# Kernel tuning notes

Hardware: AMD Instinct MI355X
Metric: run time of the kernel (lower is better)

The kernel has to match this reference:

```python
import jax, jax.numpy as jnp
import numpy as np
import math

B, S, N, D_IN = 32, 60, 25, 100
GRU, TEMB, SEMB, SEM_IN, CH, OUT, NH = 512, 512, 512, 768, 256, 512, 8


def _ln(x, g, b, eps=1e-5):
    m = jnp.mean(x, axis=-1, keepdims=True)
    v = jnp.mean((x - m) ** 2, axis=-1, keepdims=True)
    return (x - m) * jax.lax.rsqrt(v + eps) * g + b


def _gru_dir(x, w_ih, w_hh, b_ih, b_hh, reverse):
    # x: [BN, S, F]; PyTorch GRU gate order (r, z, n); returns final hidden [BN, H]
    H = w_hh.shape[1]
    gi_all = jnp.einsum('bsf,gf->bsg', x, w_ih) + b_ih  # precompute input-side gates

    def step(h, gi):
        gh = h @ w_hh.T + b_hh
        i_r, i_z, i_n = jnp.split(gi, 3, axis=-1)
        h_r, h_z, h_n = jnp.split(gh, 3, axis=-1)
        r = jax.nn.sigmoid(i_r + h_r)
        z = jax.nn.sigmoid(i_z + h_z)
        n = jnp.tanh(i_n + r * h_n)
        h_new = (1.0 - z) * n + z * h
        return h_new, None

    h0 = jnp.zeros((x.shape[0], H), x.dtype)
    h_last, _ = jax.lax.scan(step, h0, jnp.swapaxes(gi_all, 0, 1), reverse=reverse)
    return h_last


def _forward(x, seq1_w1, seq1_b1, seq1_w2, seq1_b2, ln2_g, ln2_b,
             gru_wih_f, gru_whh_f, gru_bih_f, gru_bhh_f,
             gru_wih_b, gru_whh_b, gru_bih_b, gru_bhh_b,
             ln_g, ln_b, attn_in_w, attn_in_b, fc_ta_w, fc_ta_b,
             ln3_g, ln3_b, semantic_embs, sem_w, sem_b, lnsem_g, lnsem_b,
             att_alpha, dist_adj,
             gcn_w0, gcn_b0, gcn_w1, gcn_b1, gcn_w2, gcn_b2,
             gln1_g, gln1_b, gln2_g, gln2_b,
             enc_ln_g, enc_ln_b, fc_w, fc_b):
    Bx, Sx, Nx, _ = x.shape
    # --- latent_correlation_layer ---
    xr = jnp.transpose(x, (0, 2, 1, 3)).reshape(Bx * Nx, Sx, -1)  # [BN,S,D]
    h = jax.nn.relu(xr @ seq1_w1 + seq1_b1)
    h = jax.nn.relu(h @ seq1_w2 + seq1_b2)  # dropout p=0
    h = _ln(h, ln2_g, ln2_b)  # [BN,S,512]
    hf = _gru_dir(h, gru_wih_f, gru_whh_f, gru_bih_f, gru_bhh_f, False)
    hb = _gru_dir(h, gru_wih_b, gru_whh_b, gru_bih_b, gru_bhh_b, True)
    hn = jnp.concatenate([hf, hb], axis=-1).reshape(Bx, Nx, 2 * GRU)
    hn = _ln(hn, ln_g, ln_b)  # [B,N,2*GRU]
    # multihead self-attention weights (averaged over heads, then over batch)
    hd = (2 * GRU) // NH
    qkv = hn @ attn_in_w.T + attn_in_b
    q, k, _v = jnp.split(qkv, 3, axis=-1)
    q = q.reshape(Bx, Nx, NH, hd)
    k = k.reshape(Bx, Nx, NH, hd)
    scores = jnp.einsum('bihd,bjhd->bhij', q, k) / math.sqrt(hd)
    attention = jax.nn.softmax(scores, axis=-1).mean(axis=1).mean(axis=0)  # [N,N]
    # --- node features ---
    wr = jax.nn.relu(hn @ fc_ta_w + fc_ta_b)
    X = _ln(wr, ln3_g, ln3_b)  # [B,N,TEMB]
    te = _ln(semantic_embs @ sem_w + sem_b, lnsem_g, lnsem_b)  # [N,SEMB]
    X = jnp.concatenate([X, jnp.broadcast_to(te, (Bx,) + te.shape)], axis=-1)  # [B,N,TEMB+SEMB]
    # cosine-similarity embedding attention (same for every batch element)
    en = te / jnp.maximum(jnp.linalg.norm(te, axis=-1, keepdims=True), 1e-8)
    embed_att = en @ en.T  # [N,N]
    attention = (att_alpha * dist_adj + (1.0 - att_alpha) * embed_att) * attention
    # case-amplification mask (detached in the original -> stop_gradient)
    m = jax.lax.stop_gradient(attention)
    m = jnp.maximum(m, 0.0) ** 2.5
    m = m / jnp.max(m)
    mask = (m >= 0.08).astype(x.dtype)
    adj = attention * mask
    # --- GCN block (GCNConv, add_self_loops=False, normalize=False, dense adjacency) ---
    def gcn(Xin, W, b):
        # out[i] = sum_j adj[j,i] * (Xin[j] @ W) + b  (source->target flow)
        return jnp.einsum('ji,bjf->bif', adj, Xin @ W) + b
    Xg = jax.nn.relu(gcn(X, gcn_w0, gcn_b0))
    Xg = jax.nn.relu(_ln(gcn(Xg, gcn_w1, gcn_b1) + Xg, gln1_g, gln1_b))
    Xg = jax.nn.relu(_ln(gcn(Xg, gcn_w2, gcn_b2) + Xg, gln2_g, gln2_b))
    # --- encoder head ---
    Xg = _ln(Xg, enc_ln_g, enc_ln_b)
    X_hat = jax.nn.relu(jnp.concatenate([X, Xg], axis=-1) @ fc_w + fc_b)  # [B,N,OUT]
    return X_hat


def setup_inputs():
    key = jax.random.key(0)
    c = [0]

    def nrm(shape, scale=1.0):
        c[0] += 1
        return (jax.random.normal(jax.random.fold_in(key, c[0]), shape) * scale).astype(jnp.float32)

    z = lambda *s: jnp.zeros(s, jnp.float32)
    o = lambda *s: jnp.ones(s, jnp.float32)
    FDIM = TEMB + SEMB
    d = {
        'x': nrm((B, S, N, D_IN)),
        'seq1_w1': nrm((D_IN, 256), 0.06), 'seq1_b1': z(256),
        'seq1_w2': nrm((256, 512), 0.05), 'seq1_b2': z(512),
        'ln2_g': o(512), 'ln2_b': z(512),
        'gru_wih_f': nrm((3 * GRU, 512), 0.04), 'gru_whh_f': nrm((3 * GRU, GRU), 0.04),
        'gru_bih_f': z(3 * GRU), 'gru_bhh_f': z(3 * GRU),
        'gru_wih_b': nrm((3 * GRU, 512), 0.04), 'gru_whh_b': nrm((3 * GRU, GRU), 0.04),
        'gru_bih_b': z(3 * GRU), 'gru_bhh_b': z(3 * GRU),
        'ln_g': o(2 * GRU), 'ln_b': z(2 * GRU),
        'attn_in_w': nrm((3 * 2 * GRU, 2 * GRU), 0.03), 'attn_in_b': z(3 * 2 * GRU),
        'fc_ta_w': nrm((2 * GRU, TEMB), 0.04), 'fc_ta_b': z(TEMB),
        'ln3_g': o(TEMB), 'ln3_b': z(TEMB),
        'semantic_embs': nrm((N, SEM_IN)),
        'sem_w': nrm((SEM_IN, SEMB), 0.04), 'sem_b': z(SEMB),
        'lnsem_g': o(SEMB), 'lnsem_b': z(SEMB),
        'att_alpha': jnp.float32(0.5),
        'dist_adj': jax.random.uniform(jax.random.fold_in(key, 1000), (N, N), jnp.float32),
        'gcn_w0': nrm((FDIM, CH), 0.04), 'gcn_b0': z(CH),
        'gcn_w1': nrm((CH, CH), 0.06), 'gcn_b1': z(CH),
        'gcn_w2': nrm((CH, CH), 0.06), 'gcn_b2': z(CH),
        'gln1_g': o(CH), 'gln1_b': z(CH),
        'gln2_g': o(CH), 'gln2_b': z(CH),
        'enc_ln_g': o(CH), 'enc_ln_b': z(CH),
        'fc_w': nrm((FDIM + CH, OUT), 0.04), 'fc_b': z(OUT),
    }
    return d


def reference(x, seq1_w1, seq1_b1, seq1_w2, seq1_b2, ln2_g, ln2_b,
              gru_wih_f, gru_whh_f, gru_bih_f, gru_bhh_f,
              gru_wih_b, gru_whh_b, gru_bih_b, gru_bhh_b,
              ln_g, ln_b, attn_in_w, attn_in_b, fc_ta_w, fc_ta_b,
              ln3_g, ln3_b, semantic_embs, sem_w, sem_b, lnsem_g, lnsem_b,
              att_alpha, dist_adj,
              gcn_w0, gcn_b0, gcn_w1, gcn_b1, gcn_w2, gcn_b2,
              gln1_g, gln1_b, gln2_g, gln2_b,
              enc_ln_g, enc_ln_b, fc_w, fc_b):
    return _forward(x, seq1_w1, seq1_b1, seq1_w2, seq1_b2, ln2_g, ln2_b,
                    gru_wih_f, gru_whh_f, gru_bih_f, gru_bhh_f,
                    gru_wih_b, gru_whh_b, gru_bih_b, gru_bhh_b,
                    ln_g, ln_b, attn_in_w, attn_in_b, fc_ta_w, fc_ta_b,
                    ln3_g, ln3_b, semantic_embs, sem_w, sem_b, lnsem_g, lnsem_b,
                    att_alpha, dist_adj,
                    gcn_w0, gcn_b0, gcn_w1, gcn_b1, gcn_w2, gcn_b2,
                    gln1_g, gln1_b, gln2_g, gln2_b,
                    enc_ln_g, enc_ln_b, fc_w, fc_b)
```

## Files before the change

### kernel.cpp

```cpp
#include <hip/hip_runtime.h>
#include <hip/hip_bf16.h>
#include <math.h>

#define BB 32
#define SS 60
#define NN_ 25
#define DIN 100
#define BN 800
#define GRU_H 512
#define FDIM 1024
#define CH 256
#define OUTD 512

typedef unsigned short ushort_t;
typedef float f32x4 __attribute__((ext_vector_type(4)));
typedef __bf16 bf16x8 __attribute__((ext_vector_type(8)));
typedef short s16x8 __attribute__((ext_vector_type(8)));

static const size_t O_HSEQB = 0;
static const size_t O_WB    = 12288000;
static const size_t O_HF32  = 13860864;
static const size_t O_HBB   = 15499264;
static const size_t O_HN    = 16318464;
static const size_t O_QKV   = 17137664;
static const size_t O_SC    = 18776064;
static const size_t O_ADJ   = 18939904;
static const size_t O_WR    = 18940544;
static const size_t O_TEP   = 19350144;
static const size_t O_TE    = 19362944;
static const size_t O_XCAT  = 19375744;
static const size_t O_GTMP  = 20399744;
static const size_t O_XG0   = 20604544;
static const size_t O_XG1   = 20809344;
static const size_t O_XG2   = 21014144;
static const size_t O_W1TB  = 21218944;
static const size_t O_W2TB  = 21235328;
static const size_t O_AWB   = 21300864;
static const size_t O_FTWB  = 22349440;
static const size_t O_SMWB  = 22611584;
static const size_t O_G0WB  = 22808192;
static const size_t O_G1WB  = 22939264;
static const size_t O_G2WB  = 22972032;
static const size_t O_FCWB  = 23004800;

__device__ __forceinline__ ushort_t f2b(float v)
{
  __hip_bfloat16 b = __float2bfloat16(v);
  return *reinterpret_cast<ushort_t*>(&b);
}

__device__ __forceinline__ float sig_fast(float v)
{
  return 1.f / (1.f + __expf(-v));
}
__device__ __forceinline__ float tanh_fast(float v)
{
  return 1.f - 2.f / (1.f + __expf(2.f * v));
}

__device__ __forceinline__ void block_reduce2(float& s, float& q, float* scratch)
{
  __syncthreads();
  #pragma unroll
  for (int off = 32; off > 0; off >>= 1) {
    s += __shfl_down(s, off);
    q += __shfl_down(q, off);
  }
  int tid = threadIdx.x;
  int w = tid >> 6;
  if ((tid & 63) == 0) { scratch[w * 2] = s; scratch[w * 2 + 1] = q; }
  __syncthreads();
  if (tid == 0) {
    float ss = 0.f, qq = 0.f;
    int nw = blockDim.x >> 6;
    for (int i = 0; i < nw; i++) { ss += scratch[i * 2]; qq += scratch[i * 2 + 1]; }
    scratch[0] = ss; scratch[1] = qq;
  }
  __syncthreads();
  s = scratch[0]; q = scratch[1];
}

__global__ __launch_bounds__(256) void k_cvt_w(
    const float* __restrict__ wih_f, const float* __restrict__ whh_f,
    const float* __restrict__ wih_b, const float* __restrict__ whh_b,
    ushort_t* __restrict__ wb)
{
  int i = blockIdx.x * 256 + threadIdx.x;
  wb[i]           = f2b(wih_f[i]);
  wb[786432 + i]  = f2b(whh_f[i]);
  wb[1572864 + i] = f2b(wih_b[i]);
  wb[2359296 + i] = f2b(whh_b[i]);
}

__global__ __launch_bounds__(256) void k_cvt_plain(
    const float* __restrict__ src, ushort_t* __restrict__ dst, int count)
{
  int i = blockIdx.x * 256 + threadIdx.x;
  if (i < count) dst[i] = f2b(src[i]);
}

__global__ __launch_bounds__(256) void k_cvt_t(
    const float* __restrict__ src, ushort_t* __restrict__ dst,
    int K, int N, int KP)
{
  __shared__ float tile[32][33];
  int tx = threadIdx.x & 31, ty = threadIdx.x >> 5;
  int n0 = blockIdx.x * 32, k0 = blockIdx.y * 32;
  #pragma unroll
  for (int i = 0; i < 4; i++) {
    int k = k0 + ty + i * 8, n = n0 + tx;
    tile[ty + i * 8][tx] = (k < K && n < N) ? src[(size_t)k * N + n] : 0.f;
  }
  __syncthreads();
  #pragma unroll
  for (int i = 0; i < 4; i++) {
    int n = n0 + ty + i * 8, k = k0 + tx;
    if (n < N && k < KP) dst[(size_t)n * KP + k] = f2b(tile[tx][ty + i * 8]);
  }
}

__global__ __launch_bounds__(256, 1) void k_mlp_fused(
    const float* __restrict__ x,
    const ushort_t* __restrict__ w1tb,
    const float* __restrict__ b1,
    const ushort_t* __restrict__ w2tb,
    const float* __restrict__ b2,
    const float* __restrict__ g, const float* __restrict__ be,
    ushort_t* __restrict__ hseqb)
{
  __shared__ __align__(16) ushort_t xb[64][136];
  __shared__ __align__(16) ushort_t Bl[512][40];
  __shared__ __align__(16) ushort_t h1[64][264];
  const int tid = threadIdx.x;
  const int r0 = blockIdx.x * 64;

  {
    int rr = tid >> 2;
    int d0 = (tid & 3) * 32;
    int r = r0 + rr;
    int bn = r / SS, s = r % SS;
    int b = bn / NN_, n = bn % NN_;
    const float* xp = x + (((size_t)b * SS + s) * NN_ + n) * DIN;
    ushort_t tmp[32];
    #pragma unroll
    for (int i = 0; i < 32; i++) {
      int d = d0 + i;
      tmp[i] = (d < DIN) ? f2b(xp[d]) : (ushort_t)0;
    }
    #pragma unroll
    for (int i = 0; i < 4; i++)
      *reinterpret_cast<s16x8*>(&xb[rr][d0 + i * 8]) = *reinterpret_cast<s16x8*>(&tmp[i * 8]);
  }
  const int wid = tid >> 6, l = tid & 63, lr = l & 15, lg = l >> 4;
  const int srow = tid >> 2, skg = (tid & 3) * 8;

  f32x4 acc1[16] = {};
  for (int kc = 0; kc < 4; kc++) {
    __syncthreads();
    #pragma unroll
    for (int i = 0; i < 4; i++) {
      int row = srow + i * 64;
      *reinterpret_cast<s16x8*>(&Bl[row][skg]) =
          *reinterpret_cast<const s16x8*>(w1tb + (size_t)row * 128 + kc * 32 + skg);
    }
    __syncthreads();
    bf16x8 aF = *reinterpret_cast<const bf16x8*>(&xb[wid * 16 + lr][kc * 32 + lg * 8]);
    #pragma unroll
    for (int ni = 0; ni < 16; ni++) {
      bf16x8 bF = *reinterpret_cast<const bf16x8*>(&Bl[ni * 16 + lr][lg * 8]);
      acc1[ni] = __builtin_amdgcn_mfma_f32_16x16x32_bf16(aF, bF, acc1[ni], 0, 0, 0);
    }
  }
  #pragma unroll
  for (int ni = 0; ni < 16; ni++) {
    #pragma unroll
    for (int r = 0; r < 4; r++) {
      int row = wid * 16 + lg * 4 + r;
      int col = ni * 16 + lr;
      h1[row][col] = f2b(fmaxf(acc1[ni][r] + b1[col], 0.f));
    }
  }

  f32x4 acc2[32] = {};
  for (int kc = 0; kc < 8; kc++) {
    __syncthreads();
    #pragma unroll
    for (int i = 0; i < 8; i++) {
      int row = srow + i * 64;
      *reinterpret_cast<s16x8*>(&Bl[row][skg]) =
          *reinterpret_cast<const s16x8*>(w2tb + (size_t)row * 256 + kc * 32 + skg);
    }
    __syncthreads();
    bf16x8 aF = *reinterpret_cast<const bf16x8*>(&h1[wid * 16 + lr][kc * 32 + lg * 8]);
    #pragma unroll
    for (int ni = 0; ni < 32; ni++) {
      bf16x8 bF = *reinterpret_cast<const bf16x8*>(&Bl[ni * 16 + lr][lg * 8]);
      acc2[ni] = __builtin_amdgcn_mfma_f32_16x16x32_bf16(aF, bF, acc2[ni], 0, 0, 0);
    }
  }

  float su[4] = {0.f, 0.f, 0.f, 0.f}, sq[4] = {0.f, 0.f, 0.f, 0.f};
  #pragma unroll
  for (int ni = 0; ni < 32; ni++) {
    float bb = b2[ni * 16 + lr];
    #pragma unroll
    for (int r = 0; r < 4; r++) {
      float v = fmaxf(acc2[ni][r] + bb, 0.f);
      acc2[ni][r] = v;
      su[r] += v; sq[r] += v * v;
    }
  }
  #pragma unroll
  for (int off = 1; off < 16; off <<= 1) {
    #pragma unroll
    for (int r = 0; r < 4; r++) {
      su[r] += __shfl_xor(su[r], off);
      sq[r] += __shfl_xor(sq[r], off);
    }
  }
  #pragma unroll
  for (int r = 0; r < 4; r++) {
    float mean = su[r] * (1.f / 512.f);
    float var = sq[r] * (1.f / 512.f) - mean * mean;
    float rs = rsqrtf(var + 1e-5f);
    int rowg = r0 + wid * 16 + lg * 4 + r;
    ushort_t* outp = hseqb + (size_t)rowg * 512;
    #pragma unroll
    for (int ni = 0; ni < 32; ni++) {
      int col = ni * 16 + lr;
      outp[col] = f2b((acc2[ni][r] - mean) * rs * g[col] + be[col]);
    }
  }
}

__global__ __launch_bounds__(256) void k_gru_mfma(
    const ushort_t* __restrict__ hseqb, const ushort_t* __restrict__ wb,
    const float* __restrict__ bih_f, const float* __restrict__ bhh_f,
    const float* __restrict__ bih_b, const float* __restrict__ bhh_b,
    float* __restrict__ hf32, ushort_t* __restrict__ hbb, int t)
{
  __shared__ __align__(16) ushort_t Xs[2][64][40];
  __shared__ __align__(16) ushort_t Hs[2][64][40];
  __shared__ __align__(16) ushort_t Ws[2][6][64][40];

  const int bid = blockIdx.x;
  const int xslot = bid & 7;
  const int ii = bid >> 3;
  const int pair = (ii < 13) ? xslot : (xslot + 8);
  const int mt = (ii < 13) ? ii : (ii - 13);
  const int dir = pair >> 3;
  const int jt = pair & 7;
  const int j0g = jt * 64;
  const int m0g = mt * 64;

  const ushort_t* __restrict__ wih = wb + (size_t)dir * 1572864;
  const ushort_t* __restrict__ whh = wih + 786432;
  const float* __restrict__ bih = dir ? bih_b : bih_f;
  const float* __restrict__ bhh = dir ? bhh_b : bhh_f;
  const int xt = dir ? (SS - 1 - t) : t;
  const size_t par0 = (size_t)(t & 1) * 819200 + (size_t)dir * 409600;
  const size_t par1 = (size_t)((t + 1) & 1) * 819200 + (size_t)dir * 409600;
  const float* __restrict__ hprevf = hf32 + par0;
  float* __restrict__ hnewf = hf32 + par1;
  const ushort_t* __restrict__ hprevb = hbb + par0;
  ushort_t* __restrict__ hnewb = hbb + par1;

  const int tid = threadIdx.x;
  const int srow = tid >> 2;
  const int skg = (tid & 3) * 8;
  const int smg = m0g + srow;
  const int smg_c = (smg < BN) ? smg : 0;

  const ushort_t* __restrict__ px = hseqb + ((size_t)smg_c * SS + xt) * 512 + skg;
  const ushort_t* __restrict__ ph = hprevb + (size_t)smg_c * 512 + skg;
  const ushort_t* pw[6];
  #pragma unroll
  for (int tt = 0; tt < 6; tt++) {
    const ushort_t* src = (tt < 3) ? wih : whh;
    int gate = (tt < 3) ? tt : tt - 3;
    int jglob = gate * 512 + j0g + srow;
    pw[tt] = src + (size_t)jglob * 512 + skg;
  }

  const int wid = tid >> 6;
  const int l = tid & 63;
  const int lr = l & 15;
  const int lg = l >> 4;
  const int mbase = (wid >> 1) * 32;
  const int nbase = (wid & 1) * 32;

  f32x4 accr[2][2] = {};
  f32x4 accz[2][2] = {};
  f32x4 accin[2][2] = {};
  f32x4 acchn[2][2] = {};

  s16x8 rx = *reinterpret_cast<const s16x8*>(px);
  s16x8 rh = *reinterpret_cast<const s16x8*>(ph);
  s16x8 rw[6];
  #pragma unroll
  for (int tt = 0; tt < 6; tt++) rw[tt] = *reinterpret_cast<const s16x8*>(pw[tt]);
  *reinterpret_cast<s16x8*>(&Xs[0][srow][skg]) = rx;
  *reinterpret_cast<s16x8*>(&Hs[0][srow][skg]) = rh;
  #pragma unroll
  for (int tt = 0; tt < 6; tt++) *reinterpret_cast<s16x8*>(&Ws[0][tt][srow][skg]) = rw[tt];
  __syncthreads();

  for (int it = 0; it < 16; ++it) {
    const int cur = it & 1;
    if (it < 15) {
      const int k0 = (it + 1) * 32;
      rx = *reinterpret_cast<const s16x8*>(px + k0);
      rh = *reinterpret_cast<const s16x8*>(ph + k0);
      #pragma unroll
      for (int tt = 0; tt < 6; tt++) rw[tt] = *reinterpret_cast<const s16x8*>(pw[tt] + k0);
    }

    bf16x8 xA[2], hA[2];
    #pragma unroll
    for (int mi = 0; mi < 2; mi++) {
      xA[mi] = *reinterpret_cast<const bf16x8*>(&Xs[cur][mbase + mi * 16 + lr][lg * 8]);
      hA[mi] = *reinterpret_cast<const bf16x8*>(&Hs[cur][mbase + mi * 16 + lr][lg * 8]);
    }
    #pragma unroll
    for (int ni = 0; ni < 2; ni++) {
      const int wrow = nbase + ni * 16 + lr;
      bf16x8 bWr = *reinterpret_cast<const bf16x8*>(&Ws[cur][0][wrow][lg * 8]);
      bf16x8 bWz = *reinterpret_cast<const bf16x8*>(&Ws[cur][1][wrow][lg * 8]);
      bf16x8 bWn = *reinterpret_cast<const bf16x8*>(&Ws[cur][2][wrow][lg * 8]);
      bf16x8 bVr = *reinterpret_cast<const bf16x8*>(&Ws[cur][3][wrow][lg * 8]);
      bf16x8 bVz = *reinterpret_cast<const bf16x8*>(&Ws[cur][4][wrow][lg * 8]);
      bf16x8 bVn = *reinterpret_cast<const bf16x8*>(&Ws[cur][5][wrow][lg * 8]);
      #pragma unroll
      for (int mi = 0; mi < 2; mi++) {
        accr[mi][ni]  = __builtin_amdgcn_mfma_f32_16x16x32_bf16(xA[mi], bWr, accr[mi][ni], 0, 0, 0);
        accr[mi][ni]  = __builtin_amdgcn_mfma_f32_16x16x32_bf16(hA[mi], bVr, accr[mi][ni], 0, 0, 0);
        accz[mi][ni]  = __builtin_amdgcn_mfma_f32_16x16x32_bf16(xA[mi], bWz, accz[mi][ni], 0, 0, 0);
        accz[mi][ni]  = __builtin_amdgcn_mfma_f32_16x16x32_bf16(hA[mi], bVz, accz[mi][ni], 0, 0, 0);
        accin[mi][ni] = __builtin_amdgcn_mfma_f32_16x16x32_bf16(xA[mi], bWn, accin[mi][ni], 0, 0, 0);
        acchn[mi][ni] = __builtin_amdgcn_mfma_f32_16x16x32_bf16(hA[mi], bVn, acchn[mi][ni], 0, 0, 0);
      }
    }

    if (it < 15) {
      const int nxt = cur ^ 1;
      *reinterpret_cast<s16x8*>(&Xs[nxt][srow][skg]) = rx;
      *reinterpret_cast<s16x8*>(&Hs[nxt][srow][skg]) = rh;
      #pragma unroll
      for (int tt = 0; tt < 6; tt++) *reinterpret_cast<s16x8*>(&Ws[nxt][tt][srow][skg]) = rw[tt];
    }
    __syncthreads();
  }

  #pragma unroll
  for (int mi = 0; mi < 2; mi++) {
    #pragma unroll
    for (int r = 0; r < 4; r++) {
      int m = m0g + mbase + mi * 16 + lg * 4 + r;
      if (m >= BN) continue;
      #pragma unroll
      for (int ni = 0; ni < 2; ni++) {
        int j = j0g + nbase + ni * 16 + lr;
        float sr = accr[mi][ni][r] + bih[j] + bhh[j];
        float sz = accz[mi][ni][r] + bih[512 + j] + bhh[512 + j];
        float rg = sig_fast(sr);
        float zg = sig_fast(sz);
        float ng = tanh_fast(accin[mi][ni][r] + bih[1024 + j] + rg * (acchn[mi][ni][r] + bhh[1024 + j]));
        float hp = hprevf[(size_t)m * 512 + j];
        float hvv = (1.f - zg) * ng + zg * hp;
        hnewf[(size_t)m * 512 + j] = hvv;
        hnewb[(size_t)m * 512 + j] = f2b(hvv);
      }
    }
  }
}

__global__ __launch_bounds__(256) void k_ln_hn(
    const float* __restrict__ hf, const float* __restrict__ hb,
    const float* __restrict__ g, const float* __restrict__ be,
    float* __restrict__ hn)
{
  __shared__ float scratch[8];
  int row = blockIdx.x, tid = threadIdx.x;
  float v[4];
  float s = 0.f, q = 0.f;
  #pragma unroll
  for (int p = 0; p < 4; p++) {
    int c = p * 256 + tid;
    float val = (c < 512) ? hf[(size_t)row * 512 + c] : hb[(size_t)row * 512 + (c - 512)];
    v[p] = val; s += val; q += val * val;
  }
  block_reduce2(s, q, scratch);
  float mean = s * (1.f / 1024.f);
  float var = q * (1.f / 1024.f) - mean * mean;
  float rs = rsqrtf(var + 1e-5f);
  #pragma unroll
  for (int p = 0; p < 4; p++) {
    int c = p * 256 + tid;
    hn[(size_t)row * 1024 + c] = (v[p] - mean) * rs * g[c] + be[c];
  }
}

template<int ACT>
__global__ __launch_bounds__(256) void k_bgemm(
    const float* __restrict__ A, const ushort_t* __restrict__ B,
    const float* __restrict__ bias, float* __restrict__ C,
    int M, int N, int K, int lda, int ldc)
{
  __shared__ __align__(16) ushort_t Al[64][40];
  __shared__ __align__(16) ushort_t Bl[64][40];
  const int tid = threadIdx.x;
  const int n0g = blockIdx.x * 64, m0g = blockIdx.y * 64;
  const int srow = tid >> 2, skg = (tid & 3) * 8;
  const int smg = (m0g + srow < M) ? (m0g + srow) : (M - 1);
  const int sng = (n0g + srow < N) ? (n0g + srow) : (N - 1);
  const float* pa = A + (size_t)smg * lda + skg;
  const ushort_t* pb = B + (size_t)sng * K + skg;
  const int wid = tid >> 6, l = tid & 63, lr = l & 15, lg = l >> 4;
  const int mbase = (wid >> 1) * 32, nbase = (wid & 1) * 32;
  f32x4 acc[2][2] = {};

  for (int k0 = 0; k0 < K; k0 += 32) {
    float4 a0 = *reinterpret_cast<const float4*>(pa + k0);
    float4 a1 = *reinterpret_cast<const float4*>(pa + k0 + 4);
    s16x8 bv = *reinterpret_cast<const s16x8*>(pb + k0);
    ushort_t tmp[8] = {f2b(a0.x), f2b(a0.y), f2b(a0.z), f2b(a0.w),
                       f2b(a1.x), f2b(a1.y), f2b(a1.z), f2b(a1.w)};
    *reinterpret_cast<s16x8*>(&Al[srow][skg]) = *reinterpret_cast<s16x8*>(tmp);
    *reinterpret_cast<s16x8*>(&Bl[srow][skg]) = bv;
    __syncthreads();
    bf16x8 aF[2], bF[2];
    #pragma unroll
    for (int mi = 0; mi < 2; mi++)
      aF[mi] = *reinterpret_cast<const bf16x8*>(&Al[mbase + mi * 16 + lr][lg * 8]);
    #pragma unroll
    for (int ni = 0; ni < 2; ni++)
      bF[ni] = *reinterpret_cast<const bf16x8*>(&Bl[nbase + ni * 16 + lr][lg * 8]);
    #pragma unroll
    for (int mi = 0; mi < 2; mi++)
      #pragma unroll
      for (int ni = 0; ni < 2; ni++)
        acc[mi][ni] = __builtin_amdgcn_mfma_f32_16x16x32_bf16(aF[mi], bF[ni], acc[mi][ni], 0, 0, 0);
    __syncthreads();
  }
  #pragma unroll
  for (int mi = 0; mi < 2; mi++) {
    #pragma unroll
    for (int r = 0; r < 4; r++) {
      int mg = m0g + mbase + mi * 16 + lg * 4 + r;
      if (mg >= M) continue;
      #pragma unroll
      for (int ni = 0; ni < 2; ni++) {
        int ng = n0g + nbase + ni * 16 + lr;
        if (ng >= N) continue;
        float v = acc[mi][ni][r] + (bias ? bias[ng] : 0.f);
        if (ACT == 1) v = fmaxf(v, 0.f);
        C[(size_t)mg * ldc + ng] = v;
      }
    }
  }
}

__global__ __launch_bounds__(256) void k_scores(const float* __restrict__ qkv,
                                                float* __restrict__ sc)
{
  int b = blockIdx.x, h = blockIdx.y;
  __shared__ float qs[25][128];
  __shared__ float ks[25][129];
  __shared__ float ps[25][26];
  int tid = threadIdx.x;
  for (int idx = tid; idx < 3200; idx += 256) {
    int i = idx >> 7, d = idx & 127;
    const float* base = qkv + (size_t)(b * 25 + i) * 2048 + h * 128 + d;
    qs[i][d] = base[0];
    ks[i][d] = base[1024];
  }
  __syncthreads();
  const float scale = 0.08838834764831845f;
  for (int e = tid; e < 625; e += 256) {
    int i = e / 25, j = e % 25;
    float s = 0.f;
    for (int d = 0; d < 128; d++) s += qs[i][d] * ks[j][d];
    ps[i][j] = s * scale;
  }
  __syncthreads();
  if (tid < 25) {
    float mx = -1e30f;
    for (int j = 0; j < 25; j++) mx = fmaxf(mx, ps[tid][j]);
    float s = 0.f;
    for (int j = 0; j < 25; j++) { float ev = expf(ps[tid][j] - mx); ps[tid][j] = ev; s += ev; }
    float inv = 1.f / s;
    for (int j = 0; j < 25; j++) ps[tid][j] *= inv;
  }
  __syncthreads();
  float* out = sc + (size_t)(b * 8 + h) * 640;
  for (int e = tid; e < 625; e += 256) out[e] = ps[e / 25][e % 25];
}

template<int PER>
__global__ __launch_bounds__(256) void k_ln_rows(
    const float* __restrict__ src, float* __restrict__ dst,
    const float* __restrict__ g, const float* __restrict__ be,
    int dstStride, int dstOff)
{
  __shared__ float scratch[8];
  int row = blockIdx.x, tid = threadIdx.x;
  const int C = PER * 256;
  float v[PER];
  float s = 0.f, q = 0.f;
  #pragma unroll
  for (int p = 0; p < PER; p++) {
    v[p] = src[(size_t)row * C + p * 256 + tid];
    s += v[p]; q += v[p] * v[p];
  }
  block_reduce2(s, q, scratch);
  float mean = s / (float)C;
  float var = q / (float)C - mean * mean;
  float rs = rsqrtf(var + 1e-5f);
  #pragma unroll
  for (int p = 0; p < PER; p++) {
    int c = p * 256 + tid;
    dst[(size_t)row * dstStride + dstOff + c] = (v[p] - mean) * rs * g[c] + be[c];
  }
}

__global__ __launch_bounds__(256) void k_bcast_te(const float* __restrict__ te,
                                                  float* __restrict__ xcat)
{
  int row = blockIdx.x, tid = threadIdx.x;
  int n = row % 25;
  xcat[(size_t)row * 1280 + 512 + tid] = te[n * 512 + tid];
  xcat[(size_t)row * 1280 + 768 + tid] = te[n * 512 + 256 + tid];
}

__global__ __launch_bounds__(256) void k_adj(
    const float* __restrict__ sc, const float* __restrict__ te,
    const float* __restrict__ alpha_p, const float* __restrict__ dist,
    float* __restrict__ adj)
{
  __shared__ float als[625];
  __shared__ float ninv[25];
  __shared__ float scratch[8];
  __shared__ float mxs;
  int tid = threadIdx.x;

  for (int e = tid; e < 625; e += 256) {
    float s = 0.f;
    for (int gq = 0; gq < 256; gq++) s += sc[(size_t)gq * 640 + e];
    als[e] = s * (1.f / 256.f);
  }
  if (tid < 25) {
    float s = 0.f;
    const float* tp = te + tid * 512;
    for (int d = 0; d < 512; d++) s += tp[d] * tp[d];
    ninv[tid] = 1.f / fmaxf(sqrtf(s), 1e-8f);
  }
  __syncthreads();
  float alpha = alpha_p[0];
  for (int e = tid; e < 625; e += 256) {
    int i = e / 25, j = e % 25;
    float dt = 0.f;
    const float* ti = te + i * 512;
    const float* tj = te + j * 512;
    for (int d = 0; d < 512; d++) dt += ti[d] * tj[d];
    float emb = dt * ninv[i] * ninv[j];
    als[e] = (alpha * dist[e] + (1.f - alpha) * emb) * als[e];
  }
  __syncthreads();
  float lm = 0.f;
  for (int e = tid; e < 625; e += 256) {
    float a = fmaxf(als[e], 0.f);
    lm = fmaxf(lm, powf(a, 2.5f));
  }
  #pragma unroll
  for (int off = 32; off > 0; off >>= 1) lm = fmaxf(lm, __shfl_down(lm, off));
  int w = tid >> 6;
  if ((tid & 63) == 0) scratch[w] = lm;
  __syncthreads();
  if (tid == 0) {
    float m2 = scratch[0];
    for (int i = 1; i < 4; i++) m2 = fmaxf(m2, scratch[i]);
    mxs = m2;
  }
  __syncthreads();
  float mx = mxs;
  for (int e = tid; e < 625; e += 256) {
    float a = als[e];
    float m = powf(fmaxf(a, 0.f), 2.5f) / mx;
    adj[e] = (m >= 0.08f) ? a : 0.f;
  }
}

template<int RESID, int LNORM>
__global__ __launch_bounds__(256) void k_mix(
    const float* __restrict__ adj, const float* __restrict__ tmp,
    const float* __restrict__ bias, const float* __restrict__ resid,
    const float* __restrict__ g, const float* __restrict__ be,
    float* __restrict__ out)
{
  __shared__ float adjs[25];
  __shared__ float scratch[8];
  int row = blockIdx.x;
  int b = row / 25, i = row % 25;
  int f = threadIdx.x;
  if (f < 25) adjs[f] = adj[f * 25 + i];
  __syncthreads();
  float acc = bias[f];
  const float* tp = tmp + (size_t)b * 25 * 256 + f;
  #pragma unroll 5
  for (int j = 0; j < 25; j++) acc += adjs[j] * tp[(size_t)j * 256];
  if (RESID) acc += resid[(size_t)row * 256 + f];
  float v = acc;
  if (LNORM) {
    float s = v, q = v * v;
    block_reduce2(s, q, scratch);
    float mean = s * (1.f / 256.f);
    float var = q * (1.f / 256.f) - mean * mean;
    v = (v - mean) * rsqrtf(var + 1e-5f) * g[f] + be[f];
  }
  out[(size_t)row * 256 + f] = fmaxf(v, 0.f);
}

extern "C" void kernel_launch(void* const* d_in, const int* in_sizes, int n_in,
                              void* d_out, int out_size, void* d_ws, size_t ws_size,
                              hipStream_t stream)
{
  (void)in_sizes; (void)n_in; (void)out_size; (void)ws_size;

  const float* x         = (const float*)d_in[0];
  const float* seq1_w1   = (const float*)d_in[1];
  const float* seq1_b1   = (const float*)d_in[2];
  const float* seq1_w2   = (const float*)d_in[3];
  const float* seq1_b2   = (const float*)d_in[4];
  const float* ln2_g     = (const float*)d_in[5];
  const float* ln2_b     = (const float*)d_in[6];
  const float* gru_wih_f = (const float*)d_in[7];
  const float* gru_whh_f = (const float*)d_in[8];
  const float* gru_bih_f = (const float*)d_in[9];
  const float* gru_bhh_f = (const float*)d_in[10];
  const float* gru_wih_b = (const float*)d_in[11];
  const float* gru_whh_b = (const float*)d_in[12];
  const float* gru_bih_b = (const float*)d_in[13];
  const float* gru_bhh_b = (const float*)d_in[14];
  const float* ln_g      = (const float*)d_in[15];
  const float* ln_b      = (const float*)d_in[16];
  const float* attn_in_w = (const float*)d_in[17];
  const float* attn_in_b = (const float*)d_in[18];
  const float* fc_ta_w   = (const float*)d_in[19];
  const float* fc_ta_b   = (const float*)d_in[20];
  const float* ln3_g     = (const float*)d_in[21];
  const float* ln3_b     = (const float*)d_in[22];
  const float* sem_embs  = (const float*)d_in[23];
  const float* sem_w     = (const float*)d_in[24];
  const float* sem_b     = (const float*)d_in[25];
  const float* lnsem_g   = (const float*)d_in[26];
  const float* lnsem_b   = (const float*)d_in[27];
  const float* att_alpha = (const float*)d_in[28];
  const float* dist_adj  = (const float*)d_in[29];
  const float* gcn_w0    = (const float*)d_in[30];
  const float* gcn_b0    = (const float*)d_in[31];
  const float* gcn_w1    = (const float*)d_in[32];
  const float* gcn_b1    = (const float*)d_in[33];
  const float* gcn_w2    = (const float*)d_in[34];
  const float* gcn_b2    = (const float*)d_in[35];
  const float* gln1_g    = (const float*)d_in[36];
  const float* gln1_b    = (const float*)d_in[37];
  const float* gln2_g    = (const float*)d_in[38];
  const float* gln2_b    = (const float*)d_in[39];
  const float* enc_ln_g  = (const float*)d_in[40];
  const float* enc_ln_b  = (const float*)d_in[41];
  const float* fc_w      = (const float*)d_in[42];
  const float* fc_b      = (const float*)d_in[43];

  float* w = (float*)d_ws;
  ushort_t* hseqb = (ushort_t*)(w + O_HSEQB);
  ushort_t* wb    = (ushort_t*)(w + O_WB);
  float* hf32 = w + O_HF32;
  ushort_t* hbb = (ushort_t*)(w + O_HBB);
  float* hn   = w + O_HN;
  float* qkv  = w + O_QKV;
  float* sc   = w + O_SC;
  float* adjw = w + O_ADJ;
  float* wr   = w + O_WR;
  float* tep  = w + O_TEP;
  float* te   = w + O_TE;
  float* xcat = w + O_XCAT;
  float* gtmp = w + O_GTMP;
  float* xg0  = w + O_XG0;
  float* xg1  = w + O_XG1;
  float* xg2  = w + O_XG2;
  ushort_t* w1tb = (ushort_t*)(w + O_W1TB);
  ushort_t* w2tb = (ushort_t*)(w + O_W2TB);
  ushort_t* awb  = (ushort_t*)(w + O_AWB);
  ushort_t* ftwb = (ushort_t*)(w + O_FTWB);
  ushort_t* smwb = (ushort_t*)(w + O_SMWB);
  ushort_t* g0wb = (ushort_t*)(w + O_G0WB);
  ushort_t* g1wb = (ushort_t*)(w + O_G1WB);
  ushort_t* g2wb = (ushort_t*)(w + O_G2WB);
  ushort_t* fcwb = (ushort_t*)(w + O_FCWB);

  hipMemsetAsync(hf32, 0, (size_t)819200 * sizeof(float), stream);
  hipMemsetAsync(hbb, 0, (size_t)819200 * sizeof(ushort_t), stream);

  k_cvt_w<<<3072, 256, 0, stream>>>(gru_wih_f, gru_whh_f, gru_wih_b, gru_whh_b, wb);
  k_cvt_t<<<dim3(8, 4), 256, 0, stream>>>(seq1_w1, w1tb, 100, 256, 128);
  k_cvt_t<<<dim3(16, 8), 256, 0, stream>>>(seq1_w2, w2tb, 256, 512, 256);
  k_cvt_plain<<<8192, 256, 0, stream>>>(attn_in_w, awb, 2048 * 1024);
  k_cvt_t<<<dim3(16, 32), 256, 0, stream>>>(fc_ta_w, ftwb, 1024, 512, 1024);
  k_cvt_t<<<dim3(16, 24), 256, 0, stream>>>(sem_w, smwb, 768, 512, 768);
  k_cvt_t<<<dim3(8, 32), 256, 0, stream>>>(gcn_w0, g0wb, 1024, 256, 1024);
  k_cvt_t<<<dim3(8, 8), 256, 0, stream>>>(gcn_w1, g1wb, 256, 256, 256);
  k_cvt_t<<<dim3(8, 8), 256, 0, stream>>>(gcn_w2, g2wb, 256, 256, 256);
  k_cvt_t<<<dim3(16, 40), 256, 0, stream>>>(fc_w, fcwb, 1280, 512, 1280);

  k_mlp_fused<<<750, 256, 0, stream>>>(x, w1tb, seq1_b1, w2tb, seq1_b2,
                                       ln2_g, ln2_b, hseqb);

  for (int t = 0; t < SS; t++) {
    k_gru_mfma<<<208, 256, 0, stream>>>(
        hseqb, wb, gru_bih_f, gru_bhh_f, gru_bih_b, gru_bhh_b, hf32, hbb, t);
  }

  k_ln_hn<<<800, 256, 0, stream>>>(hf32, hf32 + 409600, ln_g, ln_b, hn);

  k_bgemm<0><<<dim3(32, 13), 256, 0, stream>>>(
      hn, awb, attn_in_b, qkv, 800, 2048, 1024, 1024, 2048);

  k_scores<<<dim3(32, 8), 256, 0, stream>>>(qkv, sc);

  k_bgemm<0><<<dim3(8, 1), 256, 0, stream>>>(
      sem_embs, smwb, sem_b, tep, 25, 512, 768, 768, 512);
  k_ln_rows<2><<<25, 256, 0, stream>>>(tep, te, lnsem_g, lnsem_b, 512, 0);

  k_bgemm<1><<<dim3(8, 13), 256, 0, stream>>>(
      hn, ftwb, fc_ta_b, wr, 800, 512, 1024, 1024, 512);
  k_ln_rows<2><<<800, 256, 0, stream>>>(wr, xcat, ln3_g, ln3_b, 1280, 0);
  k_bcast_te<<<800, 256, 0, stream>>>(te, xcat);

  k_adj<<<1, 256, 0, stream>>>(sc, te, att_alpha, dist_adj, adjw);

  k_bgemm<0><<<dim3(4, 13), 256, 0, stream>>>(
      xcat, g0wb, nullptr, gtmp, 800, 256, 1024, 1280, 256);
  k_mix<0, 0><<<800, 256, 0, stream>>>(adjw, gtmp, gcn_b0, nullptr, nullptr, nullptr, xg0);
  k_bgemm<0><<<dim3(4, 13), 256, 0, stream>>>(
      xg0, g1wb, nullptr, gtmp, 800, 256, 256, 256, 256);
  k_mix<1, 1><<<800, 256, 0, stream>>>(adjw, gtmp, gcn_b1, xg0, gln1_g, gln1_b, xg1);
  k_bgemm<0><<<dim3(4, 13), 256, 0, stream>>>(
      xg1, g2wb, nullptr, gtmp, 800, 256, 256, 256, 256);
  k_mix<1, 1><<<800, 256, 0, stream>>>(adjw, gtmp, gcn_b2, xg1, gln2_g, gln2_b, xg2);

  k_ln_rows<1><<<800, 256, 0, stream>>>(xg2, xcat, enc_ln_g, enc_ln_b, 1280, 1024);

  k_bgemm<1><<<dim3(8, 13), 256, 0, stream>>>(
      xcat, fcwb, fc_b, (float*)d_out, 800, 512, 1280, 1280, 512);
}
```

Measured before the change: 1.737 ms.

## Make GRU persistent with grid barrier, batch weight conversions, widen adjacency kernel

```diff
diff --git a/kernel.cpp b/kernel.cpp
--- a/kernel.cpp
+++ b/kernel.cpp
@@ -42,6 +42,7 @@
 static const size_t O_G1WB  = 22939264;
 static const size_t O_G2WB  = 22972032;
 static const size_t O_FCWB  = 23004800;
+static const size_t O_BAR   = 23332480;
 
 __device__ __forceinline__ ushort_t f2b(float v)
 {
@@ -80,42 +81,56 @@
   s = scratch[0]; q = scratch[1];
 }
 
-__global__ __launch_bounds__(256) void k_cvt_w(
+__global__ __launch_bounds__(256) void k_cvt_plain_all(
     const float* __restrict__ wih_f, const float* __restrict__ whh_f,
     const float* __restrict__ wih_b, const float* __restrict__ whh_b,
-    ushort_t* __restrict__ wb)
+    const float* __restrict__ attn_w,
+    ushort_t* __restrict__ wb, ushort_t* __restrict__ awb)
 {
   int i = blockIdx.x * 256 + threadIdx.x;
   wb[i]           = f2b(wih_f[i]);
   wb[786432 + i]  = f2b(whh_f[i]);
   wb[1572864 + i] = f2b(wih_b[i]);
   wb[2359296 + i] = f2b(whh_b[i]);
-}
-
-__global__ __launch_bounds__(256) void k_cvt_plain(
-    const float* __restrict__ src, ushort_t* __restrict__ dst, int count)
-{
-  int i = blockIdx.x * 256 + threadIdx.x;
-  if (i < count) dst[i] = f2b(src[i]);
-}
-
-__global__ __launch_bounds__(256) void k_cvt_t(
-    const float* __restrict__ src, ushort_t* __restrict__ dst,
-    int K, int N, int KP)
+  awb[i]          = f2b(attn_w[i]);
+  awb[786432 + i] = f2b(attn_w[786432 + i]);
+  int j = 1572864 + i;
+  if (j < 2097152) awb[j] = f2b(attn_w[j]);
+}
+
+struct TJob {
+  const float* src; ushort_t* dst;
+  int K, N, KP, base;
+};
+
+__global__ __launch_bounds__(256) void k_cvt_t_all(
+    TJob j0, TJob j1, TJob j2, TJob j3, TJob j4, TJob j5, TJob j6, TJob j7)
 {
   __shared__ float tile[32][33];
+  int t = blockIdx.x;
+  TJob jb = j0;
+  if (t >= j7.base) jb = j7;
+  else if (t >= j6.base) jb = j6;
+  else if (t >= j5.base) jb = j5;
+  else if (t >= j4.base) jb = j4;
+  else if (t >= j3.base) jb = j3;
+  else if (t >= j2.base) jb = j2;
+  else if (t >= j1.base) jb = j1;
+  int local = t - jb.base;
+  int ktiles = (jb.KP + 31) >> 5;
+  int n0 = (local / ktiles) * 32;
+  int k0 = (local % ktiles) * 32;
   int tx = threadIdx.x & 31, ty = threadIdx.x >> 5;
-  int n0 = blockIdx.x * 32, k0 = blockIdx.y * 32;
   #pragma unroll
   for (int i = 0; i < 4; i++) {
     int k = k0 + ty + i * 8, n = n0 + tx;
-    tile[ty + i * 8][tx] = (k < K && n < N) ? src[(size_t)k * N + n] : 0.f;
+    tile[ty + i * 8][tx] = (k < jb.K && n < jb.N) ? jb.src[(size_t)k * jb.N + n] : 0.f;
   }
   __syncthreads();
   #pragma unroll
   for (int i = 0; i < 4; i++) {
     int n = n0 + ty + i * 8, k = k0 + tx;
-    if (n < N && k < KP) dst[(size_t)n * KP + k] = f2b(tile[tx][ty + i * 8]);
+    if (n < jb.N && k < jb.KP) jb.dst[(size_t)n * jb.KP + k] = f2b(tile[tx][ty + i * 8]);
   }
 }
 
@@ -233,11 +248,31 @@
   }
 }
 
-__global__ __launch_bounds__(256) void k_gru_mfma(
+__device__ __forceinline__ void grid_bar(int* cnt, int* sense, int nb, int target)
+{
+  __syncthreads();
+  if (threadIdx.x == 0) {
+    __threadfence();
+    int prev = __hip_atomic_fetch_add(cnt, 1, __ATOMIC_ACQ_REL, __HIP_MEMORY_SCOPE_AGENT);
+    if (prev == nb - 1) {
+      __hip_atomic_store(cnt, 0, __ATOMIC_RELAXED, __HIP_MEMORY_SCOPE_AGENT);
+      __hip_atomic_store(sense, target, __ATOMIC_RELEASE, __HIP_MEMORY_SCOPE_AGENT);
+    } else {
+      while (__hip_atomic_load(sense, __ATOMIC_ACQUIRE, __HIP_MEMORY_SCOPE_AGENT) < target) {
+        __builtin_amdgcn_s_sleep(2);
+      }
+    }
+    __threadfence();
+  }
+  __syncthreads();
+}
+
+__global__ __launch_bounds__(256, 1) void k_gru_persist(
     const ushort_t* __restrict__ hseqb, const ushort_t* __restrict__ wb,
     const float* __restrict__ bih_f, const float* __restrict__ bhh_f,
     const float* __restrict__ bih_b, const float* __restrict__ bhh_b,
-    float* __restrict__ hf32, ushort_t* __restrict__ hbb, int t)
+    float* __restrict__ hf32, ushort_t* __restrict__ hbb,
+    int* __restrict__ bar)
 {
   __shared__ __align__(16) ushort_t Xs[2][64][40];
   __shared__ __align__(16) ushort_t Hs[2][64][40];
@@ -257,13 +292,7 @@
   const ushort_t* __restrict__ whh = wih + 786432;
   const float* __restrict__ bih = dir ? bih_b : bih_f;
   const float* __restrict__ bhh = dir ? bhh_b : bhh_f;
-  const int xt = dir ? (SS - 1 - t) : t;
-  const size_t par0 = (size_t)(t & 1) * 819200 + (size_t)dir * 409600;
-  const size_t par1 = (size_t)((t + 1) & 1) * 819200 + (size_t)dir * 409600;
-  const float* __restrict__ hprevf = hf32 + par0;
-  float* __restrict__ hnewf = hf32 + par1;
-  const ushort_t* __restrict__ hprevb = hbb + par0;
-  ushort_t* __restrict__ hnewb = hbb + par1;
+  const size_t dirOff = (size_t)dir * 409600;
 
   const int tid = threadIdx.x;
   const int srow = tid >> 2;
@@ -271,8 +300,6 @@
   const int smg = m0g + srow;
   const int smg_c = (smg < BN) ? smg : 0;
 
-  const ushort_t* __restrict__ px = hseqb + ((size_t)smg_c * SS + xt) * 512 + skg;
-  const ushort_t* __restrict__ ph = hprevb + (size_t)smg_c * 512 + skg;
   const ushort_t* pw[6];
   #pragma unroll
   for (int tt = 0; tt < 6; tt++) {
@@ -289,88 +316,112 @@
   const int mbase = (wid >> 1) * 32;
   const int nbase = (wid & 1) * 32;
 
-  f32x4 accr[2][2] = {};
-  f32x4 accz[2][2] = {};
-  f32x4 accin[2][2] = {};
-  f32x4 acchn[2][2] = {};
-
-  s16x8 rx = *reinterpret_cast<const s16x8*>(px);
-  s16x8 rh = *reinterpret_cast<const s16x8*>(ph);
-  s16x8 rw[6];
-  #pragma unroll
-  for (int tt = 0; tt < 6; tt++) rw[tt] = *reinterpret_cast<const s16x8*>(pw[tt]);
-  *reinterpret_cast<s16x8*>(&Xs[0][srow][skg]) = rx;
-  *reinterpret_cast<s16x8*>(&Hs[0][srow][skg]) = rh;
-  #pragma unroll
-  for (int tt = 0; tt < 6; tt++) *reinterpret_cast<s16x8*>(&Ws[0][tt][srow][skg]) = rw[tt];
-  __syncthreads();
-
-  for (int it = 0; it < 16; ++it) {
-    const int cur = it & 1;
-    if (it < 15) {
-      const int k0 = (it + 1) * 32;
-      rx = *reinterpret_cast<const s16x8*>(px + k0);
-      rh = *reinterpret_cast<const s16x8*>(ph + k0);
-      #pragma unroll
-      for (int tt = 0; tt < 6; tt++) rw[tt] = *reinterpret_cast<const s16x8*>(pw[tt] + k0);
-    }
-
-    bf16x8 xA[2], hA[2];
-    #pragma unroll
-    for (int mi = 0; mi < 2; mi++) {
-      xA[mi] = *reinterpret_cast<const bf16x8*>(&Xs[cur][mbase + mi * 16 + lr][lg * 8]);
-      hA[mi] = *reinterpret_cast<const bf16x8*>(&Hs[cur][mbase + mi * 16 + lr][lg * 8]);
-    }
-    #pragma unroll
-    for (int ni = 0; ni < 2; ni++) {
-      const int wrow = nbase + ni * 16 + lr;
-      bf16x8 bWr = *reinterpret_cast<const bf16x8*>(&Ws[cur][0][wrow][lg * 8]);
-      bf16x8 bWz = *reinterpret_cast<const bf16x8*>(&Ws[cur][1][wrow][lg * 8]);
-      bf16x8 bWn = *reinterpret_cast<const bf16x8*>(&Ws[cur][2][wrow][lg * 8]);
-      bf16x8 bVr = *reinterpret_cast<const bf16x8*>(&Ws[cur][3][wrow][lg * 8]);
-      bf16x8 bVz = *reinterpret_cast<const bf16x8*>(&Ws[cur][4][wrow][lg * 8]);
-      bf16x8 bVn = *reinterpret_cast<const bf16x8*>(&Ws[cur][5][wrow][lg * 8]);
+  float rbr[2], rbz[2], rbin[2], rbhn[2];
+  #pragma unroll
+  for (int ni = 0; ni < 2; ni++) {
+    int j = j0g + nbase + ni * 16 + lr;
+    rbr[ni]  = bih[j] + bhh[j];
+    rbz[ni]  = bih[512 + j] + bhh[512 + j];
+    rbin[ni] = bih[1024 + j];
+    rbhn[ni] = bhh[1024 + j];
+  }
+
+  for (int t = 0; t < SS; ++t) {
+    const int xt = dir ? (SS - 1 - t) : t;
+    const size_t par0 = (size_t)(t & 1) * 819200 + dirOff;
+    const size_t par1 = (size_t)((t + 1) & 1) * 819200 + dirOff;
+    const float* __restrict__ hprevf = hf32 + par0;
+    float* __restrict__ hnewf = hf32 + par1;
+    const ushort_t* __restrict__ hprevb = hbb + par0;
+    ushort_t* __restrict__ hnewb = hbb + par1;
+    const ushort_t* __restrict__ px = hseqb + ((size_t)smg_c * SS + xt) * 512 + skg;
+    const ushort_t* __restrict__ ph = hprevb + (size_t)smg_c * 512 + skg;
+
+    f32x4 accr[2][2] = {};
+    f32x4 accz[2][2] = {};
+    f32x4 accin[2][2] = {};
+    f32x4 acchn[2][2] = {};
+
+    s16x8 rx = *reinterpret_cast<const s16x8*>(px);
+    s16x8 rh = *reinterpret_cast<const s16x8*>(ph);
+    s16x8 rw[6];
+    #pragma unroll
+    for (int tt = 0; tt < 6; tt++) rw[tt] = *reinterpret_cast<const s16x8*>(pw[tt]);
+    *reinterpret_cast<s16x8*>(&Xs[0][srow][skg]) = rx;
+    *reinterpret_cast<s16x8*>(&Hs[0][srow][skg]) = rh;
+    #pragma unroll
+    for (int tt = 0; tt < 6; tt++) *reinterpret_cast<s16x8*>(&Ws[0][tt][srow][skg]) = rw[tt];
+    __syncthreads();
+
+    for (int it = 0; it < 16; ++it) {
+      const int cur = it & 1;
+      if (it < 15) {
+        const int k0 = (it + 1) * 32;
+        rx = *reinterpret_cast<const s16x8*>(px + k0);
+        rh = *reinterpret_cast<const s16x8*>(ph + k0);
+        #pragma unroll
+        for (int tt = 0; tt < 6; tt++) rw[tt] = *reinterpret_cast<const s16x8*>(pw[tt] + k0);
+      }
+
+      bf16x8 xA[2], hA[2];
       #pragma unroll
       for (int mi = 0; mi < 2; mi++) {
-        accr[mi][ni]  = __builtin_amdgcn_mfma_f32_16x16x32_bf16(xA[mi], bWr, accr[mi][ni], 0, 0, 0);
-        accr[mi][ni]  = __builtin_amdgcn_mfma_f32_16x16x32_bf16(hA[mi], bVr, accr[mi][ni], 0, 0, 0);
-        accz[mi][ni]  = __builtin_amdgcn_mfma_f32_16x16x32_bf16(xA[mi], bWz, accz[mi][ni], 0, 0, 0);
-        accz[mi][ni]  = __builtin_amdgcn_mfma_f32_16x16x32_bf16(hA[mi], bVz, accz[mi][ni], 0, 0, 0);
-        accin[mi][ni] = __builtin_amdgcn_mfma_f32_16x16x32_bf16(xA[mi], bWn, accin[mi][ni], 0, 0, 0);
-        acchn[mi][ni] = __builtin_amdgcn_mfma_f32_16x16x32_bf16(hA[mi], bVn, acchn[mi][ni], 0, 0, 0);
+        xA[mi] = *reinterpret_cast<const bf16x8*>(&Xs[cur][mbase + mi * 16 + lr][lg * 8]);
+        hA[mi] = *reinterpret_cast<const bf16x8*>(&Hs[cur][mbase + mi * 16 + lr][lg * 8]);
       }
-    }
-
-    if (it < 15) {
-      const int nxt = cur ^ 1;
-      *reinterpret_cast<s16x8*>(&Xs[nxt][srow][skg]) = rx;
-      *reinterpret_cast<s16x8*>(&Hs[nxt][srow][skg]) = rh;
-      #pragma unroll
-      for (int tt = 0; tt < 6; tt++) *reinterpret_cast<s16x8*>(&Ws[nxt][tt][srow][skg]) = rw[tt];
-    }
-    __syncthreads();
-  }
-
-  #pragma unroll
-  for (int mi = 0; mi < 2; mi++) {
-    #pragma unroll
-    for (int r = 0; r < 4; r++) {
-      int m = m0g + mbase + mi * 16 + lg * 4 + r;
-      if (m >= BN) continue;
       #pragma unroll
       for (int ni = 0; ni < 2; ni++) {
-        int j = j0g + nbase + ni * 16 + lr;
-        float sr = accr[mi][ni][r] + bih[j] + bhh[j];
-        float sz = accz[mi][ni][r] + bih[512 + j] + bhh[512 + j];
-        float rg = sig_fast(sr);
-        float zg = sig_fast(sz);
-        float ng = tanh_fast(accin[mi][ni][r] + bih[1024 + j] + rg * (acchn[mi][ni][r] + bhh[1024 + j]));
-        float hp = hprevf[(size_t)m * 512 + j];
-        float hvv = (1.f - zg) * ng + zg * hp;
-        hnewf[(size_t)m * 512 + j] = hvv;
-        hnewb[(size_t)m * 512 + j] = f2b(hvv);
+        const int wrow = nbase + ni * 16 + lr;
+        bf16x8 bWr = *reinterpret_cast<const bf16x8*>(&Ws[cur][0][wrow][lg * 8]);
+        bf16x8 bWz = *reinterpret_cast<const bf16x8*>(&Ws[cur][1][wrow][lg * 8]);
+        bf16x8 bWn = *reinterpret_cast<const bf16x8*>(&Ws[cur][2][wrow][lg * 8]);
+        bf16x8 bVr = *reinterpret_cast<const bf16x8*>(&Ws[cur][3][wrow][lg * 8]);
+        bf16x8 bVz = *reinterpret_cast<const bf16x8*>(&Ws[cur][4][wrow][lg * 8]);
+        bf16x8 bVn = *reinterpret_cast<const bf16x8*>(&Ws[cur][5][wrow][lg * 8]);
+        #pragma unroll
+        for (int mi = 0; mi < 2; mi++) {
+          accr[mi][ni]  = __builtin_amdgcn_mfma_f32_16x16x32_bf16(xA[mi], bWr, accr[mi][ni], 0, 0, 0);
+          accr[mi][ni]  = __builtin_amdgcn_mfma_f32_16x16x32_bf16(hA[mi], bVr, accr[mi][ni], 0, 0, 0);
+          accz[mi][ni]  = __builtin_amdgcn_mfma_f32_16x16x32_bf16(xA[mi], bWz, accz[mi][ni], 0, 0, 0);
+          accz[mi][ni]  = __builtin_amdgcn_mfma_f32_16x16x32_bf16(hA[mi], bVz, accz[mi][ni], 0, 0, 0);
+          accin[mi][ni] = __builtin_amdgcn_mfma_f32_16x16x32_bf16(xA[mi], bWn, accin[mi][ni], 0, 0, 0);
+          acchn[mi][ni] = __builtin_amdgcn_mfma_f32_16x16x32_bf16(hA[mi], bVn, acchn[mi][ni], 0, 0, 0);
+        }
       }
-    }
+
+      if (it < 15) {
+        const int nxt = cur ^ 1;
+        *reinterpret_cast<s16x8*>(&Xs[nxt][srow][skg]) = rx;
+        *reinterpret_cast<s16x8*>(&Hs[nxt][srow][skg]) = rh;
+        #pragma unroll
+        for (int tt = 0; tt < 6; tt++) *reinterpret_cast<s16x8*>(&Ws[nxt][tt][srow][skg]) = rw[tt];
+      }
+      __syncthreads();
+    }
+
+    #pragma unroll
+    for (int mi = 0; mi < 2; mi++) {
+      #pragma unroll
+      for (int r = 0; r < 4; r++) {
+        int m = m0g + mbase + mi * 16 + lg * 4 + r;
+        if (m >= BN) continue;
+        #pragma unroll
+        for (int ni = 0; ni < 2; ni++) {
+          int j = j0g + nbase + ni * 16 + lr;
+          float sr = accr[mi][ni][r] + rbr[ni];
+          float sz = accz[mi][ni][r] + rbz[ni];
+          float rg = sig_fast(sr);
+          float zg = sig_fast(sz);
+          float ng = tanh_fast(accin[mi][ni][r] + rbin[ni] + rg * (acchn[mi][ni][r] + rbhn[ni]));
+          float hp = hprevf[(size_t)m * 512 + j];
+          float hvv = (1.f - zg) * ng + zg * hp;
+          hnewf[(size_t)m * 512 + j] = hvv;
+          hnewb[(size_t)m * 512 + j] = f2b(hvv);
+        }
+      }
+    }
+
+    if (t < SS - 1) grid_bar(bar, bar + 1, 208, t + 1);
   }
 }
 
@@ -532,44 +583,44 @@
   xcat[(size_t)row * 1280 + 768 + tid] = te[n * 512 + 256 + tid];
 }
 
-__global__ __launch_bounds__(256) void k_adj(
+__global__ __launch_bounds__(1024) void k_adj(
     const float* __restrict__ sc, const float* __restrict__ te,
     const float* __restrict__ alpha_p, const float* __restrict__ dist,
     float* __restrict__ adj)
 {
+  __shared__ float tes[25][517];
   __shared__ float als[625];
-  __shared__ float ninv[25];
-  __shared__ float scratch[8];
+  __shared__ float dots[625];
+  __shared__ float scratch[16];
   __shared__ float mxs;
   int tid = threadIdx.x;
 
-  for (int e = tid; e < 625; e += 256) {
+  for (int idx = tid; idx < 12800; idx += 1024)
+    tes[idx >> 9][idx & 511] = te[idx];
+  __syncthreads();
+
+  if (tid < 625) {
+    int i = tid / 25, j = tid % 25;
     float s = 0.f;
-    for (int gq = 0; gq < 256; gq++) s += sc[(size_t)gq * 640 + e];
-    als[e] = s * (1.f / 256.f);
-  }
-  if (tid < 25) {
-    float s = 0.f;
-    const float* tp = te + tid * 512;
-    for (int d = 0; d < 512; d++) s += tp[d] * tp[d];
-    ninv[tid] = 1.f / fmaxf(sqrtf(s), 1e-8f);
+    for (int gq = 0; gq < 256; gq++) s += sc[(size_t)gq * 640 + tid];
+    als[tid] = s * (1.f / 256.f);
+    float dt = 0.f;
+    const float* ti = tes[i];
+    const float* tj = tes[j];
+    for (int d = 0; d < 512; d++) dt += ti[d] * tj[d];
+    dots[tid] = dt;
   }
   __syncthreads();
   float alpha = alpha_p[0];
-  for (int e = tid; e < 625; e += 256) {
-    int i = e / 25, j = e % 25;
-    float dt = 0.f;
-    const float* ti = te + i * 512;
-    const float* tj = te + j * 512;
-    for (int d = 0; d < 512; d++) dt += ti[d] * tj[d];
-    float emb = dt * ninv[i] * ninv[j];
-    als[e] = (alpha * dist[e] + (1.f - alpha) * emb) * als[e];
-  }
-  __syncthreads();
   float lm = 0.f;
-  for (int e = tid; e < 625; e += 256) {
-    float a = fmaxf(als[e], 0.f);
-    lm = fmaxf(lm, powf(a, 2.5f));
+  if (tid < 625) {
+    int i = tid / 25, j = tid % 25;
+    float ni = 1.f / fmaxf(sqrtf(dots[i * 26]), 1e-8f);
+    float nj = 1.f / fmaxf(sqrtf(dots[j * 26]), 1e-8f);
+    float emb = dots[tid] * ni * nj;
+    float a = (alpha * dist[tid] + (1.f - alpha) * emb) * als[tid];
+    als[tid] = a;
+    lm = powf(fmaxf(a, 0.f), 2.5f);
   }
   #pragma unroll
   for (int off = 32; off > 0; off >>= 1) lm = fmaxf(lm, __shfl_down(lm, off));
@@ -578,15 +629,14 @@
   __syncthreads();
   if (tid == 0) {
     float m2 = scratch[0];
-    for (int i = 1; i < 4; i++) m2 = fmaxf(m2, scratch[i]);
+    for (int i = 1; i < 16; i++) m2 = fmaxf(m2, scratch[i]);
     mxs = m2;
   }
   __syncthreads();
-  float mx = mxs;
-  for (int e = tid; e < 625; e += 256) {
-    float a = als[e];
-    float m = powf(fmaxf(a, 0.f), 2.5f) / mx;
-    adj[e] = (m >= 0.08f) ? a : 0.f;
+  if (tid < 625) {
+    float a = als[tid];
+    float m = powf(fmaxf(a, 0.f), 2.5f) / mxs;
+    adj[tid] = (m >= 0.08f) ? a : 0.f;
   }
 }
 
@@ -697,28 +747,31 @@
   ushort_t* g1wb = (ushort_t*)(w + O_G1WB);
   ushort_t* g2wb = (ushort_t*)(w + O_G2WB);
   ushort_t* fcwb = (ushort_t*)(w + O_FCWB);
+  int* bar = (int*)(w + O_BAR);
 
   hipMemsetAsync(hf32, 0, (size_t)819200 * sizeof(float), stream);
   hipMemsetAsync(hbb, 0, (size_t)819200 * sizeof(ushort_t), stream);
-
-  k_cvt_w<<<3072, 256, 0, stream>>>(gru_wih_f, gru_whh_f, gru_wih_b, gru_whh_b, wb);
-  k_cvt_t<<<dim3(8, 4), 256, 0, stream>>>(seq1_w1, w1tb, 100, 256, 128);
-  k_cvt_t<<<dim3(16, 8), 256, 0, stream>>>(seq1_w2, w2tb, 256, 512, 256);
-  k_cvt_plain<<<8192, 256, 0, stream>>>(attn_in_w, awb, 2048 * 1024);
-  k_cvt_t<<<dim3(16, 32), 256, 0, stream>>>(fc_ta_w, ftwb, 1024, 512, 1024);
-  k_cvt_t<<<dim3(16, 24), 256, 0, stream>>>(sem_w, smwb, 768, 512, 768);
-  k_cvt_t<<<dim3(8, 32), 256, 0, stream>>>(gcn_w0, g0wb, 1024, 256, 1024);
-  k_cvt_t<<<dim3(8, 8), 256, 0, stream>>>(gcn_w1, g1wb, 256, 256, 256);
-  k_cvt_t<<<dim3(8, 8), 256, 0, stream>>>(gcn_w2, g2wb, 256, 256, 256);
-  k_cvt_t<<<dim3(16, 40), 256, 0, stream>>>(fc_w, fcwb, 1280, 512, 1280);
+  hipMemsetAsync(bar, 0, 2 * sizeof(int), stream);
+
+  k_cvt_plain_all<<<3072, 256, 0, stream>>>(gru_wih_f, gru_whh_f, gru_wih_b,
+                                            gru_whh_b, attn_in_w, wb, awb);
+  {
+    TJob j0 = {seq1_w1, w1tb, 100, 256, 128, 0};
+    TJob j1 = {seq1_w2, w2tb, 256, 512, 256, 32};
+    TJob j2 = {fc_ta_w, ftwb, 1024, 512, 1024, 160};
+    TJob j3 = {sem_w, smwb, 768, 512, 768, 672};
+    TJob j4 = {gcn_w0, g0wb, 1024, 256, 1024, 1056};
+    TJob j5 = {gcn_w1, g1wb, 256, 256, 256, 1312};
+    TJob j6 = {gcn_w2, g2wb, 256, 256, 256, 1376};
+    TJob j7 = {fc_w, fcwb, 1280, 512, 1280, 1440};
+    k_cvt_t_all<<<2080, 256, 0, stream>>>(j0, j1, j2, j3, j4, j5, j6, j7);
+  }
 
   k_mlp_fused<<<750, 256, 0, stream>>>(x, w1tb, seq1_b1, w2tb, seq1_b2,
                                        ln2_g, ln2_b, hseqb);
 
-  for (int t = 0; t < SS; t++) {
-    k_gru_mfma<<<208, 256, 0, stream>>>(
-        hseqb, wb, gru_bih_f, gru_bhh_f, gru_bih_b, gru_bhh_b, hf32, hbb, t);
-  }
+  k_gru_persist<<<208, 256, 0, stream>>>(
+      hseqb, wb, gru_bih_f, gru_bhh_f, gru_bih_b, gru_bhh_b, hf32, hbb, bar);
 
   k_ln_hn<<<800, 256, 0, stream>>>(hf32, hf32 + 409600, ln_g, ln_b, hn);
 
@@ -736,7 +789,7 @@
   k_ln_rows<2><<<800, 256, 0, stream>>>(wr, xcat, ln3_g, ln3_b, 1280, 0);
   k_bcast_te<<<800, 256, 0, stream>>>(te, xcat);
 
-  k_adj<<<1, 256, 0, stream>>>(sc, te, att_alpha, dist_adj, adjw);
+  k_adj<<<1, 1024, 0, stream>>>(sc, te, att_alpha, dist_adj, adjw);
 
   k_bgemm<0><<<dim3(4, 13), 256, 0, stream>>>(
       xcat, g0wb, nullptr, gtmp, 800, 256, 1024, 1280, 256);
```

Result: slower. 3.161 ms (+82.0%).
